# Kernel tuning notes

Hardware: AMD Instinct MI355X
Metric: run time of the kernel (lower is better)

## Reference

```python
import jax, jax.numpy as jnp
import numpy as np
import math

B, S, H, Dh, Dr, HID, C = 2, 2048, 16, 128, 64, 2048, 512

def _linear(x, w, b):
    return x @ w.T + b

def _rope(x):
    # x: [B, H, S, Dr]; interleaved-pair rotation as in the torch module
    d = x.shape[-1]
    s = x.shape[2]
    inv_freq = 1.0 / (10000.0 ** (jnp.arange(0, d, 2, dtype=jnp.float32) / d))
    sinusoid = jnp.arange(s, dtype=jnp.float32)[:, None] * inv_freq[None, :]  # [S, d/2]
    sin, cos = jnp.sin(sinusoid), jnp.cos(sinusoid)  # broadcast over B,H
    x1 = x[..., 0::2]
    x2 = x[..., 1::2]
    rot = jnp.stack([x1 * cos - x2 * sin, x1 * sin + x2 * cos], axis=-1)
    return rot.reshape(x.shape)

def setup_inputs() -> dict:
    key = jax.random.key(0)
    ks = jax.random.split(key, 9)
    sc = 0.02
    return {
        "x": jax.random.normal(ks[0], (B, S, HID), jnp.float32),
        "d_kv_w": jax.random.normal(ks[1], (C, HID), jnp.float32) * sc,
        "d_kv_b": jnp.zeros((C,), jnp.float32),
        "u_k_w": jax.random.normal(ks[2], (H * Dh, C), jnp.float32) * sc,
        "u_k_b": jnp.zeros((H * Dh,), jnp.float32),
        "u_v_w": jax.random.normal(ks[3], (H * Dh, C), jnp.float32) * sc,
        "u_v_b": jnp.zeros((H * Dh,), jnp.float32),
        "d_q_w": jax.random.normal(ks[4], (C, HID), jnp.float32) * sc,
        "d_q_b": jnp.zeros((C,), jnp.float32),
        "u_q_w": jax.random.normal(ks[5], (H * Dh, C), jnp.float32) * sc,
        "u_q_b": jnp.zeros((H * Dh,), jnp.float32),
        "qr_w": jax.random.normal(ks[6], (H * Dr, C), jnp.float32) * sc,
        "qr_b": jnp.zeros((H * Dr,), jnp.float32),
        "out_w": jax.random.normal(ks[7], (HID, H * Dh), jnp.float32) * sc,
        "out_b": jnp.zeros((HID,), jnp.float32),
    }

def reference(x, d_kv_w, d_kv_b, u_k_w, u_k_b, u_v_w, u_v_b,
              d_q_w, d_q_b, u_q_w, u_q_b, qr_w, qr_b, out_w, out_b):
    b, s, _ = x.shape
    kv_c = _linear(x, d_kv_w, d_kv_b)                      # [B,S,C]
    k_c = _linear(kv_c, u_k_w, u_k_b).reshape(b, s, H, Dh)
    k_r = _linear(kv_c, qr_w, qr_b).reshape(b, s, H, Dr)   # note: qr_proj reused, as in source
    v = _linear(kv_c, u_v_w, u_v_b).reshape(b, s, H, Dh)
    q_c_lat = _linear(x, d_q_w, d_q_b)                     # [B,S,C]
    q_c = _linear(q_c_lat, u_q_w, u_q_b).reshape(b, s, H, Dh)
    q_r = _linear(q_c_lat, qr_w, qr_b).reshape(b, s, H, Dr)
    # RoPE operates on [B,H,S,Dr]
    q_r = _rope(q_r.transpose(0, 2, 1, 3)).transpose(0, 2, 1, 3)
    k_r = _rope(k_r.transpose(0, 2, 1, 3)).transpose(0, 2, 1, 3)
    q = jnp.concatenate([q_c, q_r], axis=-1)               # [B,S,H,Dh+Dr]
    k = jnp.concatenate([k_c, k_r], axis=-1)
    scale = 1.0 / math.sqrt(Dh + Dr)
    scores = jnp.einsum('bqhd,bkhd->bhqk', q, k) * scale   # [B,H,S,S]
    probs = jax.nn.softmax(scores, axis=-1)
    ctx = jnp.einsum('bhqk,bkhd->bqhd', probs, v).reshape(b, s, H * Dh)
    return _linear(ctx, out_w, out_b)
```

## Files before the change

### kernel.cpp

```cpp
#include <hip/hip_runtime.h>
#include <hip/hip_bf16.h>
#include <math.h>
#include <stdint.h>

#define NB 2
#define NS 2048
#define NH 16
#define NDH 128
#define NDR 64
#define NHID 2048
#define NC 512

typedef unsigned short u16;
typedef short short8 __attribute__((ext_vector_type(8)));
typedef short short4v __attribute__((ext_vector_type(4)));
typedef float f32x4 __attribute__((ext_vector_type(4)));

template <int V> struct IC { static constexpr int value = V; };

__device__ __forceinline__ u16 f2bf(float f) {
  union { float f; uint32_t u; } c; c.f = f;
  uint32_t u = c.u + 0x7fffu + ((c.u >> 16) & 1u);
  return (u16)(u >> 16);
}
__device__ __forceinline__ float bf2f(u16 b) {
  union { uint32_t u; float f; } c; c.u = ((uint32_t)b) << 16;
  return c.f;
}
__device__ __forceinline__ void async16(const void* g, void* l) {
  __builtin_amdgcn_global_load_lds((const __attribute__((address_space(1))) void*)g,
                                   (__attribute__((address_space(3))) void*)l, 16, 0, 0);
}
__device__ __forceinline__ uint32_t cvtpk(float a, float b) {
  uint32_t r;
  asm("v_cvt_pk_bf16_f32 %0, %1, %2" : "=v"(r) : "v"(a), "v"(b));
  return r;
}

struct CastArgs {
  const float* src[8];
  u16* dst[8];
  int start[8];
};

__global__ __launch_bounds__(256) void cast_kernel(CastArgs a) {
  int blk = blockIdx.x;
  int ti = 0;
#pragma unroll
  for (int i = 1; i < 8; ++i) ti += (blk >= a.start[i]) ? 1 : 0;
  size_t off = (size_t)(blk - a.start[ti]) * 2048 + (size_t)threadIdx.x * 8;
  const float4* s = (const float4*)(a.src[ti] + off);
  float4 v0 = s[0], v1 = s[1];
  u16 o[8];
  o[0] = f2bf(v0.x); o[1] = f2bf(v0.y); o[2] = f2bf(v0.z); o[3] = f2bf(v0.w);
  o[4] = f2bf(v1.x); o[5] = f2bf(v1.y); o[6] = f2bf(v1.z); o[7] = f2bf(v1.w);
  *(short8*)(a.dst[ti] + off) = *(short8*)o;
}

struct GemmSeg {
  const u16* A;
  const u16* W;
  const float* bias;
  void* dst;
  int K;
  int mode;
  int ldc;
};
struct GemmArgs {
  GemmSeg seg[5];
  int nbstart[6];
  int nseg;
};

__global__ __launch_bounds__(256) void gemm_bt(GemmArgs ga) {
  __shared__ char glds[32768];
  const int nb = blockIdx.x, mb = blockIdx.y;
  int si = 0;
  for (int i = 1; i < ga.nseg; ++i) si += (nb >= ga.nbstart[i]) ? 1 : 0;
  GemmSeg sg = ga.seg[si];
  const int nbl = nb - ga.nbstart[si];
  const int K = sg.K;
  const int t = threadIdx.x;
  const int l = t & 63, w = t >> 6;
  const int r0 = t >> 2, c0 = (t & 3) * 8;
  const int wm = (w >> 1) * 64, wn = (w & 1) * 64;
  const int frow = l & 15, fk = (l >> 4) * 8;
  const int lafO = ((wm + frow) * 32 + fk) * 2;
  const int lbfO = 8192 + ((wn + frow) * 32 + fk) * 2;

  const u16* apA = sg.A + (size_t)mb * 128 * K + (size_t)r0 * K + c0;
  const u16* wpA = sg.W + (size_t)nbl * 128 * K + (size_t)r0 * K + c0;

  auto stage = [&](int bufOff) {
    async16(apA, glds + bufOff + t * 16);
    async16(apA + (size_t)64 * K, glds + bufOff + 4096 + t * 16);
    async16(wpA, glds + bufOff + 8192 + t * 16);
    async16(wpA + (size_t)64 * K, glds + bufOff + 12288 + t * 16);
    apA += 32; wpA += 32;
  };

  const f32x4 vzero = {0.f, 0.f, 0.f, 0.f};
  f32x4 acc[4][4];
#pragma unroll
  for (int i = 0; i < 4; ++i)
#pragma unroll
    for (int j = 0; j < 4; ++j) acc[i][j] = vzero;

  stage(0);
  const int nk = K / 32;

  auto ktile = [&](auto bufc, bool stageNext) {
    constexpr int BO = decltype(bufc)::value;
    if (stageNext) {
      stage(BO ^ 16384);
      asm volatile("s_waitcnt vmcnt(4)" ::: "memory");
    } else {
      asm volatile("s_waitcnt vmcnt(0)" ::: "memory");
    }
    __builtin_amdgcn_s_barrier();
    asm volatile("" ::: "memory");
    short8 af[4], bfr[4];
#pragma unroll
    for (int i = 0; i < 4; ++i) af[i] = *(const short8*)(glds + BO + lafO + i * 1024);
#pragma unroll
    for (int j = 0; j < 4; ++j) bfr[j] = *(const short8*)(glds + BO + lbfO + j * 1024);
    __builtin_amdgcn_s_setprio(1);
#pragma unroll
    for (int i = 0; i < 4; ++i)
#pragma unroll
      for (int j = 0; j < 4; ++j)
        acc[i][j] = __builtin_amdgcn_mfma_f32_16x16x32_bf16(af[i], bfr[j], acc[i][j], 0, 0, 0);
    __builtin_amdgcn_s_setprio(0);
    asm volatile("s_waitcnt lgkmcnt(0)" ::: "memory");
    __builtin_amdgcn_s_barrier();
  };

  for (int kk = 0; kk < nk; kk += 2) {
    ktile(IC<0>{}, true);
    ktile(IC<16384>{}, kk + 2 < nk);
  }

  const int rb = (l >> 4) * 4;
  const int cl = l & 15;
  if (sg.mode == 0) {
    u16* D = (u16*)sg.dst;
#pragma unroll
    for (int i = 0; i < 4; ++i)
#pragma unroll
      for (int j = 0; j < 4; ++j) {
        int col = nbl * 128 + wn + j * 16 + cl;
        float bv = sg.bias[col];
#pragma unroll
        for (int r = 0; r < 4; ++r) {
          int row = mb * 128 + wm + i * 16 + rb + r;
          D[(size_t)row * sg.ldc + col] = f2bf(acc[i][j][r] + bv);
        }
      }
  } else if (sg.mode == 2) {
    float* D = (float*)sg.dst;
#pragma unroll
    for (int i = 0; i < 4; ++i)
#pragma unroll
      for (int j = 0; j < 4; ++j) {
        int col = nbl * 128 + wn + j * 16 + cl;
        float bv = sg.bias[col];
#pragma unroll
        for (int r = 0; r < 4; ++r) {
          int row = mb * 128 + wm + i * 16 + rb + r;
          D[(size_t)row * sg.ldc + col] = acc[i][j][r] + bv;
        }
      }
  } else {
    u16* D = (u16*)sg.dst;
#pragma unroll
    for (int i = 0; i < 4; ++i) {
      int row0 = mb * 128 + wm + i * 16 + rb;
      int bb = row0 >> 11, ss = row0 & (NS - 1);
#pragma unroll
      for (int j = 0; j < 4; ++j) {
        int col = nbl * 128 + wn + j * 16 + cl;
        int hh = col >> 7, dv = col & 127;
        float bv = sg.bias[col];
        u16 pk[4];
#pragma unroll
        for (int r = 0; r < 4; ++r) pk[r] = f2bf(acc[i][j][r] + bv);
        *(short4v*)(D + ((size_t)((bb * NH + hh) * NDH + dv)) * NS + ss) = *(short4v*)pk;
      }
    }
  }
}

__global__ __launch_bounds__(256) void rope_kernel(u16* kr, u16* qr) {
  int tid = blockIdx.x * 256 + threadIdx.x;
  int which = tid >> 19;
  int loc = tid & ((1 << 19) - 1);
  int row = loc >> 7;
  int ch = loc & 127;
  int s = row & (NS - 1);
  u16* p = (which ? qr : kr) + (size_t)row * (NH * NDR) + ch * 8;
  short8 v = *(short8*)p;
  int jb = (ch & 7) * 4;
  u16 o[8];
#pragma unroll
  for (int q = 0; q < 4; ++q) {
    int j = jb + q;
    float invf = exp2f(-(float)j * 0.41524101186f);
    float ang = (float)s * invf;
    float sn = sinf(ang), cs = cosf(ang);
    float x1 = bf2f(((u16*)&v)[2 * q]);
    float x2 = bf2f(((u16*)&v)[2 * q + 1]);
    o[2 * q]     = f2bf(x1 * cs - x2 * sn);
    o[2 * q + 1] = f2bf(x1 * sn + x2 * cs);
  }
  *(short8*)p = *(short8*)o;
}

__global__ __launch_bounds__(256, 2) void attn_kernel(
    const u16* __restrict__ Qc, const u16* __restrict__ Qr,
    const u16* __restrict__ Kc, const u16* __restrict__ Kr,
    const u16* __restrict__ VT, u16* __restrict__ Ctx) {
  extern __shared__ char smem[];
  const int t = threadIdx.x, w = t >> 6, l = t & 63;
  const int g = l >> 4, cl = l & 15;
  const int lin = blockIdx.x;
  const int xcd = lin & 7, idx = lin >> 3;
  const int bh = xcd * 4 + (idx >> 4);
  const int qb = idx & 15;
  const int b = bh >> 4, h = bh & 15;
  const int q0 = qb * 128 + w * 32;

  short8 qf[2][6];
#pragma unroll
  for (int qr = 0; qr < 2; ++qr) {
    const u16* qc = Qc + ((size_t)(b * NS + q0 + qr * 16 + cl)) * NHID + h * NDH + g * 8;
    const u16* qrp = Qr + ((size_t)(b * NS + q0 + qr * 16 + cl)) * (NH * NDR) + h * NDR + g * 8;
#pragma unroll
    for (int c = 0; c < 4; ++c) qf[qr][c] = *(const short8*)(qc + c * 32);
    qf[qr][4] = *(const short8*)(qrp);
    qf[qr][5] = *(const short8*)(qrp + 32);
  }
#pragma unroll
  for (int qr = 0; qr < 2; ++qr)
#pragma unroll
    for (int c = 0; c < 6; ++c) asm volatile("" :: "v"(qf[qr][c]));

  const u16* kptr[6]; int kstep[6];
#pragma unroll
  for (int r = 0; r < 6; ++r) {
    int Lb = r * 4096 + t * 16;
    int row = Lb / 384;
    int off = Lb - row * 384;
    int c = (off ^ ((row & 7) << 4)) >> 1;
    if (c < NDH) { kptr[r] = Kc + ((size_t)(b * NS + row)) * NHID + h * NDH + c; kstep[r] = 64 * NHID; }
    else { kptr[r] = Kr + ((size_t)(b * NS + row)) * (NH * NDR) + h * NDR + (c - NDH); kstep[r] = 64 * NH * NDR; }
  }
  const u16* vptr[4];
#pragma unroll
  for (int r = 0; r < 4; ++r) {
    int Lb = r * 4096 + t * 16;
    int row = Lb >> 7, off = Lb & 127;
    int c = (off ^ ((row & 7) << 4)) >> 1;
    vptr[r] = VT + ((size_t)(bh * NDH + row)) * NS + c;
  }

  const int xo = (cl & 7) << 4;
  int kaddr[6], vaddr[4];
#pragma unroll
  for (int c = 0; c < 6; ++c) kaddr[c] = cl * 384 + ((c * 64 + g * 16) ^ xo);
#pragma unroll
  for (int n = 0; n < 4; ++n) vaddr[n] = 24576 + cl * 128 + ((n * 32 + g * 8) ^ xo);

  float m2[2] = {-1e30f, -1e30f};
  float lsum[2] = {0.f, 0.f};
  const f32x4 vzero = {0.f, 0.f, 0.f, 0.f};
  f32x4 o[2][8];
#pragma unroll
  for (int qr = 0; qr < 2; ++qr)
#pragma unroll
    for (int d = 0; d < 8; ++d) o[qr][d] = vzero;
  const float scale2 = 0.10411757f;

  auto stage_into = [&](int bufOff) {
#pragma unroll
    for (int r = 0; r < 6; ++r) { async16(kptr[r], smem + bufOff + r * 4096 + t * 16); kptr[r] += kstep[r]; }
#pragma unroll
    for (int r = 0; r < 4; ++r) { async16(vptr[r], smem + bufOff + 24576 + r * 4096 + t * 16); vptr[r] += 64; }
  };
  stage_into(0);

  auto tile = [&](auto bufc, bool stageNext) {
    constexpr int BO = decltype(bufc)::value;
    if (stageNext) {
      stage_into(BO ^ 40960);
      asm volatile("s_waitcnt vmcnt(10)" ::: "memory");
    } else {
      asm volatile("s_waitcnt vmcnt(0)" ::: "memory");
    }
    __builtin_amdgcn_s_barrier();
    asm volatile("" ::: "memory");

    f32x4 sa[2][4];
#pragma unroll
    for (int qr = 0; qr < 2; ++qr)
#pragma unroll
      for (int n = 0; n < 4; ++n) sa[qr][n] = vzero;
#pragma unroll
    for (int n = 0; n < 4; ++n) {
      short8 kf[6];
#pragma unroll
      for (int c = 0; c < 6; ++c)
        kf[c] = *(const short8*)(smem + kaddr[c] + (BO + n * 6144));
      __builtin_amdgcn_s_setprio(1);
#pragma unroll
      for (int c = 0; c < 6; ++c) {
        sa[0][n] = __builtin_amdgcn_mfma_f32_16x16x32_bf16(kf[c], qf[0][c], sa[0][n], 0, 0, 0);
        sa[1][n] = __builtin_amdgcn_mfma_f32_16x16x32_bf16(kf[c], qf[1][c], sa[1][n], 0, 0, 0);
      }
      __builtin_amdgcn_s_setprio(0);
    }

    short4v pb[2][4];
#pragma unroll
    for (int qr = 0; qr < 2; ++qr) {
      float mx = fmaxf(fmaxf(sa[qr][0][0], sa[qr][0][1]), fmaxf(sa[qr][0][2], sa[qr][0][3]));
#pragma unroll
      for (int n = 1; n < 4; ++n)
        mx = fmaxf(mx, fmaxf(fmaxf(sa[qr][n][0], sa[qr][n][1]), fmaxf(sa[qr][n][2], sa[qr][n][3])));
      mx = fmaxf(mx, __shfl_xor(mx, 16));
      mx = fmaxf(mx, __shfl_xor(mx, 32));
      float mxs = mx * scale2;
      if (!__all(mxs <= m2[qr] + 6.0f)) {
        float mn = fmaxf(m2[qr], mxs);
        float sf = exp2f(m2[qr] - mn);
        m2[qr] = mn;
        lsum[qr] *= sf;
        f32x4 sfv = {sf, sf, sf, sf};
#pragma unroll
        for (int d = 0; d < 8; ++d) o[qr][d] *= sfv;
      }
      float nm = -m2[qr];
      float ps = 0.f;
#pragma unroll
      for (int n = 0; n < 4; ++n) {
        float p0 = exp2f(fmaf(sa[qr][n][0], scale2, nm));
        float p1 = exp2f(fmaf(sa[qr][n][1], scale2, nm));
        float p2 = exp2f(fmaf(sa[qr][n][2], scale2, nm));
        float p3 = exp2f(fmaf(sa[qr][n][3], scale2, nm));
        ps += (p0 + p1) + (p2 + p3);
        union { uint32_t u[2]; short4v s; } pu;
        pu.u[0] = cvtpk(p0, p1);
        pu.u[1] = cvtpk(p2, p3);
        pb[qr][n] = pu.s;
      }
      ps += __shfl_xor(ps, 16);
      ps += __shfl_xor(ps, 32);
      lsum[qr] += ps;
    }

#pragma unroll
    for (int n = 0; n < 4; ++n) {
      __builtin_amdgcn_s_setprio(1);
#pragma unroll
      for (int d = 0; d < 8; ++d) {
        short4v va = *(const short4v*)(smem + vaddr[n] + (BO + d * 2048));
        o[0][d] = __builtin_amdgcn_mfma_f32_16x16x16bf16_1k(va, pb[0][n], o[0][d], 0, 0, 0);
        o[1][d] = __builtin_amdgcn_mfma_f32_16x16x16bf16_1k(va, pb[1][n], o[1][d], 0, 0, 0);
      }
      __builtin_amdgcn_s_setprio(0);
    }

    asm volatile("s_waitcnt lgkmcnt(0)" ::: "memory");
    __builtin_amdgcn_s_barrier();
  };

  for (int kv = 0; kv < NS / 64; kv += 2) {
    tile(IC<0>{}, true);
    tile(IC<40960>{}, kv + 2 < NS / 64);
  }

#pragma unroll
  for (int qr = 0; qr < 2; ++qr) {
    float invq = 1.f / lsum[qr];
    u16* dst = Ctx + ((size_t)(b * NS + q0 + qr * 16 + cl)) * NHID + h * NDH + g * 4;
#pragma unroll
    for (int d = 0; d < 8; ++d) {
      float a0 = o[qr][d][0] * invq, a1 = o[qr][d][1] * invq;
      float a2 = o[qr][d][2] * invq, a3 = o[qr][d][3] * invq;
      union { uint32_t u[2]; short4v s; } pu;
      pu.u[0] = cvtpk(a0, a1);
      pu.u[1] = cvtpk(a2, a3);
      *(short4v*)(dst + d * 16) = pu.s;
    }
  }
}

extern "C" void kernel_launch(void* const* d_in, const int* in_sizes, int n_in,
                              void* d_out, int out_size, void* d_ws, size_t ws_size,
                              hipStream_t stream) {
  (void)in_sizes; (void)n_in; (void)out_size;
  const float* x      = (const float*)d_in[0];
  const float* d_kv_w = (const float*)d_in[1];
  const float* d_kv_b = (const float*)d_in[2];
  const float* u_k_w  = (const float*)d_in[3];
  const float* u_k_b  = (const float*)d_in[4];
  const float* u_v_w  = (const float*)d_in[5];
  const float* u_v_b  = (const float*)d_in[6];
  const float* d_q_w  = (const float*)d_in[7];
  const float* d_q_b  = (const float*)d_in[8];
  const float* u_q_w  = (const float*)d_in[9];
  const float* u_q_b  = (const float*)d_in[10];
  const float* qr_w   = (const float*)d_in[11];
  const float* qr_b   = (const float*)d_in[12];
  const float* out_w  = (const float*)d_in[13];
  const float* out_b  = (const float*)d_in[14];

  char* ws = (char*)d_ws;
  size_t off = 0;
  auto alloc = [&](size_t bytes) -> void* {
    void* p = ws + off;
    off += (bytes + 255) & ~(size_t)255;
    return p;
  };
  u16* xb   = (u16*)alloc((size_t)NB * NS * NHID * 2);
  u16* wdkv = (u16*)alloc((size_t)NC * NHID * 2);
  u16* wuk  = (u16*)alloc((size_t)NH * NDH * NC * 2);
  u16* wuv  = (u16*)alloc((size_t)NH * NDH * NC * 2);
  u16* wdq  = (u16*)alloc((size_t)NC * NHID * 2);
  u16* wuq  = (u16*)alloc((size_t)NH * NDH * NC * 2);
  u16* wqr  = (u16*)alloc((size_t)NH * NDR * NC * 2);
  u16* wout = (u16*)alloc((size_t)NHID * NH * NDH * 2);
  u16* kvc  = (u16*)alloc((size_t)NB * NS * NC * 2);
  u16* qlat = (u16*)alloc((size_t)NB * NS * NC * 2);
  u16* Kc   = (u16*)alloc((size_t)NB * NS * NH * NDH * 2);
  u16* Krt  = (u16*)alloc((size_t)NB * NS * NH * NDR * 2);
  u16* Qc   = (u16*)alloc((size_t)NB * NS * NH * NDH * 2);
  u16* Qrt  = (u16*)alloc((size_t)NB * NS * NH * NDR * 2);
  u16* VT   = (u16*)alloc((size_t)NB * NH * NDH * NS * 2);
  u16* ctx  = xb;
  if (off > ws_size) return;

  {
    CastArgs ca;
    const float* srcs[8] = {x, d_kv_w, u_k_w, u_v_w, d_q_w, u_q_w, qr_w, out_w};
    u16* dsts[8] = {xb, wdkv, wuk, wuv, wdq, wuq, wqr, wout};
    int sizes[8] = {NB * NS * NHID, NC * NHID, NH * NDH * NC, NH * NDH * NC,
                    NC * NHID, NH * NDH * NC, NH * NDR * NC, NHID * NH * NDH};
    int st = 0;
    for (int i = 0; i < 8; ++i) {
      ca.src[i] = srcs[i]; ca.dst[i] = dsts[i]; ca.start[i] = st;
      st += sizes[i] / 2048;
    }
    cast_kernel<<<dim3(st), dim3(256), 0, stream>>>(ca);
  }

  {
    GemmArgs ga;
    ga.nseg = 2;
    ga.seg[0] = {xb, wdkv, d_kv_b, kvc, NHID, 0, NC};
    ga.seg[1] = {xb, wdq,  d_q_b,  qlat, NHID, 0, NC};
    for (int i = 2; i < 5; ++i) ga.seg[i] = ga.seg[0];
    ga.nbstart[0] = 0; ga.nbstart[1] = 4; ga.nbstart[2] = 8;
    ga.nbstart[3] = 8; ga.nbstart[4] = 8; ga.nbstart[5] = 8;
    gemm_bt<<<dim3(8, 32), dim3(256), 0, stream>>>(ga);
  }

  {
    GemmArgs ga;
    ga.nseg = 5;
    ga.seg[0] = {kvc,  wuk, u_k_b, Kc,  NC, 0, NH * NDH};
    ga.seg[1] = {kvc,  wuv, u_v_b, VT,  NC, 1, 0};
    ga.seg[2] = {kvc,  wqr, qr_b,  Krt, NC, 0, NH * NDR};
    ga.seg[3] = {qlat, wuq, u_q_b, Qc,  NC, 0, NH * NDH};
    ga.seg[4] = {qlat, wqr, qr_b,  Qrt, NC, 0, NH * NDR};
    ga.nbstart[0] = 0;  ga.nbstart[1] = 16; ga.nbstart[2] = 32;
    ga.nbstart[3] = 40; ga.nbstart[4] = 56; ga.nbstart[5] = 64;
    gemm_bt<<<dim3(64, 32), dim3(256), 0, stream>>>(ga);
  }

  rope_kernel<<<dim3(4096), dim3(256), 0, stream>>>(Krt, Qrt);

  hipFuncSetAttribute((const void*)attn_kernel,
                      hipFuncAttributeMaxDynamicSharedMemorySize, 81920);
  attn_kernel<<<dim3(512), dim3(256), 81920, stream>>>(Qc, Qrt, Kc, Krt, VT, ctx);

  {
    GemmArgs ga;
    ga.nseg = 1;
    ga.seg[0] = {ctx, wout, out_b, d_out, NHID, 2, NHID};
    for (int i = 1; i < 5; ++i) ga.seg[i] = ga.seg[0];
    ga.nbstart[0] = 0;
    for (int i = 1; i < 6; ++i) ga.nbstart[i] = 16;
    gemm_bt<<<dim3(16, 32), dim3(256), 0, stream>>>(ga);
  }
}
```

Before: 303.7 us.

## Switch attention MFMAs to 32x32x16 tiles with permlane32 P transpose

Rewrites the attention inner loop to use 32x32x16 bf16 MFMAs for both QK^T and PV in place of 16x16x32 and 16x16x16 ones. Each wave now holds a single 32-query tile, so the softmax max and sum reductions need only one cross-half shuffle. The probability fragments are rearranged into B-operand layout with permlane32_swap instead of going through LDS. The goal is fewer MFMA issues, fewer LDS reads per FLOP and less shuffle overhead, at the cost of larger accumulators (64 fp32 registers), which could pressure occupancy and needs the LDS swizzle addressing to stay correct.

```diff
diff --git a/kernel.cpp b/kernel.cpp
--- a/kernel.cpp
+++ b/kernel.cpp
@@ -15,6 +15,8 @@
 typedef short short8 __attribute__((ext_vector_type(8)));
 typedef short short4v __attribute__((ext_vector_type(4)));
 typedef float f32x4 __attribute__((ext_vector_type(4)));
+typedef float f32x16 __attribute__((ext_vector_type(16)));
+typedef int int2v __attribute__((ext_vector_type(2)));
 
 template <int V> struct IC { static constexpr int value = V; };
 
@@ -31,8 +33,8 @@
   __builtin_amdgcn_global_load_lds((const __attribute__((address_space(1))) void*)g,
                                    (__attribute__((address_space(3))) void*)l, 16, 0, 0);
 }
-__device__ __forceinline__ uint32_t cvtpk(float a, float b) {
-  uint32_t r;
+__device__ __forceinline__ int cvtpk(float a, float b) {
+  int r;
   asm("v_cvt_pk_bf16_f32 %0, %1, %2" : "=v"(r) : "v"(a), "v"(b));
   return r;
 }
@@ -221,7 +223,7 @@
     const u16* __restrict__ VT, u16* __restrict__ Ctx) {
   extern __shared__ char smem[];
   const int t = threadIdx.x, w = t >> 6, l = t & 63;
-  const int g = l >> 4, cl = l & 15;
+  const int hi = l >> 5, q32 = l & 31;
   const int lin = blockIdx.x;
   const int xcd = lin & 7, idx = lin >> 3;
   const int bh = xcd * 4 + (idx >> 4);
@@ -229,20 +231,17 @@
   const int b = bh >> 4, h = bh & 15;
   const int q0 = qb * 128 + w * 32;
 
-  short8 qf[2][6];
-#pragma unroll
-  for (int qr = 0; qr < 2; ++qr) {
-    const u16* qc = Qc + ((size_t)(b * NS + q0 + qr * 16 + cl)) * NHID + h * NDH + g * 8;
-    const u16* qrp = Qr + ((size_t)(b * NS + q0 + qr * 16 + cl)) * (NH * NDR) + h * NDR + g * 8;
-#pragma unroll
-    for (int c = 0; c < 4; ++c) qf[qr][c] = *(const short8*)(qc + c * 32);
-    qf[qr][4] = *(const short8*)(qrp);
-    qf[qr][5] = *(const short8*)(qrp + 32);
-  }
-#pragma unroll
-  for (int qr = 0; qr < 2; ++qr)
-#pragma unroll
-    for (int c = 0; c < 6; ++c) asm volatile("" :: "v"(qf[qr][c]));
+  short8 qf[12];
+  {
+    const u16* qcp = Qc + ((size_t)(b * NS + q0 + q32)) * NHID + h * NDH + hi * 8;
+    const u16* qrp = Qr + ((size_t)(b * NS + q0 + q32)) * (NH * NDR) + h * NDR + hi * 8;
+#pragma unroll
+    for (int dw = 0; dw < 8; ++dw) qf[dw] = *(const short8*)(qcp + dw * 16);
+#pragma unroll
+    for (int dw = 0; dw < 4; ++dw) qf[8 + dw] = *(const short8*)(qrp + dw * 16);
+  }
+#pragma unroll
+  for (int dw = 0; dw < 12; ++dw) asm volatile("" :: "v"(qf[dw]));
 
   const u16* kptr[6]; int kstep[6];
 #pragma unroll
@@ -263,21 +262,13 @@
     vptr[r] = VT + ((size_t)(bh * NDH + row)) * NS + c;
   }
 
-  const int xo = (cl & 7) << 4;
-  int kaddr[6], vaddr[4];
-#pragma unroll
-  for (int c = 0; c < 6; ++c) kaddr[c] = cl * 384 + ((c * 64 + g * 16) ^ xo);
-#pragma unroll
-  for (int n = 0; n < 4; ++n) vaddr[n] = 24576 + cl * 128 + ((n * 32 + g * 8) ^ xo);
-
-  float m2[2] = {-1e30f, -1e30f};
-  float lsum[2] = {0.f, 0.f};
-  const f32x4 vzero = {0.f, 0.f, 0.f, 0.f};
-  f32x4 o[2][8];
-#pragma unroll
-  for (int qr = 0; qr < 2; ++qr)
-#pragma unroll
-    for (int d = 0; d < 8; ++d) o[qr][d] = vzero;
+  const int kswz = (l & 7) << 4;
+  float m2 = -1e30f, lsum = 0.f;
+  f32x16 acc[4];
+#pragma unroll
+  for (int i = 0; i < 4; ++i)
+#pragma unroll
+    for (int r = 0; r < 16; ++r) acc[i][r] = 0.f;
   const float scale2 = 0.10411757f;
 
   auto stage_into = [&](int bufOff) {
@@ -299,74 +290,73 @@
     __builtin_amdgcn_s_barrier();
     asm volatile("" ::: "memory");
 
-    f32x4 sa[2][4];
-#pragma unroll
-    for (int qr = 0; qr < 2; ++qr)
-#pragma unroll
-      for (int n = 0; n < 4; ++n) sa[qr][n] = vzero;
-#pragma unroll
-    for (int n = 0; n < 4; ++n) {
-      short8 kf[6];
-#pragma unroll
-      for (int c = 0; c < 6; ++c)
-        kf[c] = *(const short8*)(smem + kaddr[c] + (BO + n * 6144));
+    f32x16 sa[2];
+#pragma unroll
+    for (int n = 0; n < 2; ++n)
+#pragma unroll
+      for (int r = 0; r < 16; ++r) sa[n][r] = 0.f;
+#pragma unroll
+    for (int dw = 0; dw < 12; ++dw) {
+      int ko = q32 * 384 + ((dw * 32 + hi * 16) ^ kswz);
+      short8 k0 = *(const short8*)(smem + BO + ko);
+      short8 k1 = *(const short8*)(smem + BO + 12288 + ko);
       __builtin_amdgcn_s_setprio(1);
-#pragma unroll
-      for (int c = 0; c < 6; ++c) {
-        sa[0][n] = __builtin_amdgcn_mfma_f32_16x16x32_bf16(kf[c], qf[0][c], sa[0][n], 0, 0, 0);
-        sa[1][n] = __builtin_amdgcn_mfma_f32_16x16x32_bf16(kf[c], qf[1][c], sa[1][n], 0, 0, 0);
+      sa[0] = __builtin_amdgcn_mfma_f32_32x32x16_bf16(k0, qf[dw], sa[0], 0, 0, 0);
+      sa[1] = __builtin_amdgcn_mfma_f32_32x32x16_bf16(k1, qf[dw], sa[1], 0, 0, 0);
+      __builtin_amdgcn_s_setprio(0);
+    }
+
+    float mx = sa[0][0];
+#pragma unroll
+    for (int r = 1; r < 16; ++r) mx = fmaxf(mx, sa[0][r]);
+#pragma unroll
+    for (int r = 0; r < 16; ++r) mx = fmaxf(mx, sa[1][r]);
+    mx = fmaxf(mx, __shfl_xor(mx, 32));
+    float mxs = mx * scale2;
+    if (!__all(mxs <= m2 + 6.0f)) {
+      float mn = fmaxf(m2, mxs);
+      float sf = exp2f(m2 - mn);
+      m2 = mn;
+      lsum *= sf;
+#pragma unroll
+      for (int i = 0; i < 4; ++i) acc[i] *= sf;
+    }
+    float nm = -m2;
+    float ps = 0.f;
+#pragma unroll
+    for (int n = 0; n < 2; ++n)
+#pragma unroll
+      for (int r = 0; r < 16; ++r) {
+        float p = exp2f(fmaf(sa[n][r], scale2, nm));
+        sa[n][r] = p;
+        ps += p;
       }
-      __builtin_amdgcn_s_setprio(0);
-    }
-
-    short4v pb[2][4];
-#pragma unroll
-    for (int qr = 0; qr < 2; ++qr) {
-      float mx = fmaxf(fmaxf(sa[qr][0][0], sa[qr][0][1]), fmaxf(sa[qr][0][2], sa[qr][0][3]));
-#pragma unroll
-      for (int n = 1; n < 4; ++n)
-        mx = fmaxf(mx, fmaxf(fmaxf(sa[qr][n][0], sa[qr][n][1]), fmaxf(sa[qr][n][2], sa[qr][n][3])));
-      mx = fmaxf(mx, __shfl_xor(mx, 16));
-      mx = fmaxf(mx, __shfl_xor(mx, 32));
-      float mxs = mx * scale2;
-      if (!__all(mxs <= m2[qr] + 6.0f)) {
-        float mn = fmaxf(m2[qr], mxs);
-        float sf = exp2f(m2[qr] - mn);
-        m2[qr] = mn;
-        lsum[qr] *= sf;
-        f32x4 sfv = {sf, sf, sf, sf};
-#pragma unroll
-        for (int d = 0; d < 8; ++d) o[qr][d] *= sfv;
+    ps += __shfl_xor(ps, 32);
+    lsum += ps;
+
+#pragma unroll
+    for (int n = 0; n < 2; ++n) {
+#pragma unroll
+      for (int w2 = 0; w2 < 2; ++w2) {
+        const int base = w2 * 8;
+        int A0 = cvtpk(sa[n][base + 0], sa[n][base + 1]);
+        int A1 = cvtpk(sa[n][base + 2], sa[n][base + 3]);
+        int B0 = cvtpk(sa[n][base + 4], sa[n][base + 5]);
+        int B1 = cvtpk(sa[n][base + 6], sa[n][base + 7]);
+        int2v r02 = __builtin_amdgcn_permlane32_swap(A0, B0, false, false);
+        int2v r13 = __builtin_amdgcn_permlane32_swap(A1, B1, false, false);
+        union { int i[4]; short8 s; } F;
+        F.i[0] = r02[0]; F.i[1] = r13[0]; F.i[2] = r02[1]; F.i[3] = r13[1];
+        const int W = n * 2 + w2;
+        const int vo = q32 * 128 + ((W * 32 + hi * 16) ^ kswz);
+        __builtin_amdgcn_s_setprio(1);
+#pragma unroll
+        for (int d32 = 0; d32 < 4; ++d32) {
+          short8 va = *(const short8*)(smem + BO + 24576 + d32 * 4096 + vo);
+          acc[d32] = __builtin_amdgcn_mfma_f32_32x32x16_bf16(va, F.s, acc[d32], 0, 0, 0);
+        }
+        __builtin_amdgcn_s_setprio(0);
       }
-      float nm = -m2[qr];
-      float ps = 0.f;
-#pragma unroll
-      for (int n = 0; n < 4; ++n) {
-        float p0 = exp2f(fmaf(sa[qr][n][0], scale2, nm));
-        float p1 = exp2f(fmaf(sa[qr][n][1], scale2, nm));
-        float p2 = exp2f(fmaf(sa[qr][n][2], scale2, nm));
-        float p3 = exp2f(fmaf(sa[qr][n][3], scale2, nm));
-        ps += (p0 + p1) + (p2 + p3);
-        union { uint32_t u[2]; short4v s; } pu;
-        pu.u[0] = cvtpk(p0, p1);
-        pu.u[1] = cvtpk(p2, p3);
-        pb[qr][n] = pu.s;
-      }
-      ps += __shfl_xor(ps, 16);
-      ps += __shfl_xor(ps, 32);
-      lsum[qr] += ps;
-    }
-
-#pragma unroll
-    for (int n = 0; n < 4; ++n) {
-      __builtin_amdgcn_s_setprio(1);
-#pragma unroll
-      for (int d = 0; d < 8; ++d) {
-        short4v va = *(const short4v*)(smem + vaddr[n] + (BO + d * 2048));
-        o[0][d] = __builtin_amdgcn_mfma_f32_16x16x16bf16_1k(va, pb[0][n], o[0][d], 0, 0, 0);
-        o[1][d] = __builtin_amdgcn_mfma_f32_16x16x16bf16_1k(va, pb[1][n], o[1][d], 0, 0, 0);
-      }
-      __builtin_amdgcn_s_setprio(0);
     }
 
     asm volatile("s_waitcnt lgkmcnt(0)" ::: "memory");
@@ -378,20 +368,19 @@
     tile(IC<40960>{}, kv + 2 < NS / 64);
   }
 
-#pragma unroll
-  for (int qr = 0; qr < 2; ++qr) {
-    float invq = 1.f / lsum[qr];
-    u16* dst = Ctx + ((size_t)(b * NS + q0 + qr * 16 + cl)) * NHID + h * NDH + g * 4;
-#pragma unroll
-    for (int d = 0; d < 8; ++d) {
-      float a0 = o[qr][d][0] * invq, a1 = o[qr][d][1] * invq;
-      float a2 = o[qr][d][2] * invq, a3 = o[qr][d][3] * invq;
-      union { uint32_t u[2]; short4v s; } pu;
-      pu.u[0] = cvtpk(a0, a1);
-      pu.u[1] = cvtpk(a2, a3);
-      *(short4v*)(dst + d * 16) = pu.s;
-    }
-  }
+  float invq = 1.f / lsum;
+  u16* dst = Ctx + ((size_t)(b * NS + q0 + q32)) * NHID + h * NDH + hi * 4;
+#pragma unroll
+  for (int d32 = 0; d32 < 4; ++d32)
+#pragma unroll
+    for (int m2x = 0; m2x < 4; ++m2x) {
+      float a0 = acc[d32][m2x * 4 + 0] * invq, a1 = acc[d32][m2x * 4 + 1] * invq;
+      float a2 = acc[d32][m2x * 4 + 2] * invq, a3 = acc[d32][m2x * 4 + 3] * invq;
+      union { int i[2]; short4v s; } pu;
+      pu.i[0] = cvtpk(a0, a1);
+      pu.i[1] = cvtpk(a2, a3);
+      *(short4v*)(dst + d32 * 32 + m2x * 8) = pu.s;
+    }
 }
 
 extern "C" void kernel_launch(void* const* d_in, const int* in_sizes, int n_in,
```

Result: faster. 280.5 us (-7.6%).
